# Kernel tuning notes

Measured on AMD Instinct MI355X. Metric: run time of the kernel, lower is better.

Reference implementation:

```python
import jax, jax.numpy as jnp
import numpy as np

B, T, D, H, NW = 2, 2048, 1024, 16, 64
HD = D // H  # 64
EPS = 1e-12  # F.normalize eps


def setup_inputs() -> dict:
    key = jax.random.key(0)
    ks = jax.random.split(key, 8)
    def lin(k, din, dout):
        return jax.random.normal(k, (din, dout), jnp.float32) / np.sqrt(din).astype(np.float32)
    return {
        "x": jax.random.normal(ks[0], (B, T, D), jnp.float32),
        "Wqf": lin(ks[1], D, H * NW), "bqf": jnp.zeros((H * NW,), jnp.float32),
        "Wkf": lin(ks[2], D, H * NW), "bkf": jnp.zeros((H * NW,), jnp.float32),
        "Wqp": lin(ks[3], D, H * NW), "bqp": jnp.zeros((H * NW,), jnp.float32),
        "Wkp": lin(ks[4], D, H * NW), "bkp": jnp.zeros((H * NW,), jnp.float32),
        "Wv": lin(ks[5], D, D), "bv": jnp.zeros((D,), jnp.float32),
        "Wo": lin(ks[6], D, D), "bo": jnp.zeros((D,), jnp.float32),
        "scale": jnp.ones((H, 1, 1), jnp.float32),  # interference_scale
    }


def reference(x, Wqf, bqf, Wkf, bkf, Wqp, bqp, Wkp, bkp, Wv, bv, Wo, bo, scale):
    Bx, Tx, Dx = x.shape
    def heads(W, b, nd):  # [B,T,H*nd] -> [B,H,T,nd]
        return jnp.transpose((x @ W + b).reshape(Bx, Tx, H, nd), (0, 2, 1, 3))
    qf = heads(Wqf, bqf, NW); kf = heads(Wkf, bkf, NW)
    qp = heads(Wqp, bqp, NW); kp = heads(Wkp, bkp, NW)
    v = heads(Wv, bv, HD)
    t = jnp.arange(Tx, dtype=x.dtype)[None, None, :, None]  # [1,1,T,1]
    def wave_norm(f, p):
        w = jnp.sin(f * t + p)  # [B,H,T,NW]
        n = jnp.sqrt(jnp.sum(w * w, axis=-1, keepdims=True))
        return w / jnp.maximum(n, EPS)
    qn = wave_norm(qf, qp)
    kn = wave_norm(kf, kp)
    inter = jnp.einsum('bhtw,bhsw->bhts', qn, kn) * scale[None]  # [B,H,T,T]
    causal = jnp.tril(jnp.ones((Tx, Tx), bool))  # keep diag and below
    inter = jnp.where(causal, inter, jnp.zeros((), x.dtype))
    denom = jnp.sqrt(jnp.arange(1, Tx + 1, dtype=x.dtype))[:, None]  # [T,1]
    attn = inter / denom
    # dropout is identity in eval mode
    out = jnp.einsum('bhts,bhsd->bhtd', attn, v)
    out = jnp.transpose(out, (0, 2, 1, 3)).reshape(Bx, Tx, Dx)
    return out @ Wo + bo
```

## Files before the change

kernel.cpp:

```cpp
#include <hip/hip_runtime.h>


#define Bb 2
#define Tt 2048
#define Dd 1024
#define Hh 16
#define NC 32

typedef _Float16 half_t;
typedef _Float16 half8 __attribute__((ext_vector_type(8)));
typedef _Float16 half4h __attribute__((ext_vector_type(4)));
typedef float f32x16 __attribute__((ext_vector_type(16)));

#define MFMA32(a, b, c) __builtin_amdgcn_mfma_f32_32x32x16_f16((a), (b), (c), 0, 0, 0)

#define GLL(G, L) __builtin_amdgcn_global_load_lds(                      \
    (const __attribute__((address_space(1))) void*)(G),                  \
    (__attribute__((address_space(3))) void*)(L), 16, 0, 0)

__global__ __launch_bounds__(256) void xsplit_kernel(
    const float* __restrict__ X, half_t* __restrict__ XHI, half_t* __restrict__ XLO)
{
  const size_t i = ((size_t)blockIdx.x * 256 + threadIdx.x) * 8;
  float4 a = *(const float4*)&X[i];
  float4 b = *(const float4*)&X[i + 4];
  const float av[8] = {a.x, a.y, a.z, a.w, b.x, b.y, b.z, b.w};
  half8 hv, lv;
  #pragma unroll
  for (int j = 0; j < 8; ++j) {
    half_t hx = (half_t)av[j];
    hv[j] = hx; lv[j] = (half_t)((av[j] - (float)hx) * 2048.f);
  }
  *(half8*)&XHI[i] = hv;
  *(half8*)&XLO[i] = lv;
}

__global__ __launch_bounds__(256) void wsplit_kernel(
    const float* __restrict__ W0, const float* __restrict__ W1,
    const float* __restrict__ W2, const float* __restrict__ W3,
    const float* __restrict__ W4, const float* __restrict__ W5,
    half_t* __restrict__ WSP)
{
  __shared__ float Ld[64][68];
  const int tid = threadIdx.x;
  const int m = blockIdx.z;
  const float* W = (m == 0) ? W0 : (m == 1) ? W1 : (m == 2) ? W2
                 : (m == 3) ? W3 : (m == 4) ? W4 : W5;
  const int k0 = blockIdx.x * 64, n0 = blockIdx.y * 64;
  const int r = tid >> 2, c4 = (tid & 3) * 16;
  #pragma unroll
  for (int i = 0; i < 4; ++i)
    *(float4*)&Ld[r][c4 + i * 4] =
        *(const float4*)&W[(size_t)(k0 + r) * Dd + n0 + c4 + i * 4];
  __syncthreads();
  half_t* hi = WSP + (size_t)m * 2097152;
  half_t* lo = hi + 1048576;
  const int n = tid >> 2, kc = (tid & 3) * 16;
  half8 hv0, hv1, lv0, lv1;
  #pragma unroll
  for (int i = 0; i < 8; ++i) {
    float v0 = Ld[kc + i][n];
    half_t h0 = (half_t)v0;
    hv0[i] = h0; lv0[i] = (half_t)((v0 - (float)h0) * 2048.f);
    float v1 = Ld[kc + 8 + i][n];
    half_t h1 = (half_t)v1;
    hv1[i] = h1; lv1[i] = (half_t)((v1 - (float)h1) * 2048.f);
  }
  *(half8*)&hi[(size_t)(n0 + n) * Dd + k0 + kc]     = hv0;
  *(half8*)&hi[(size_t)(n0 + n) * Dd + k0 + kc + 8] = hv1;
  *(half8*)&lo[(size_t)(n0 + n) * Dd + k0 + kc]     = lv0;
  *(half8*)&lo[(size_t)(n0 + n) * Dd + k0 + kc + 8] = lv1;
}

__global__ __launch_bounds__(256, 2) void proj_kernel(
    const half_t* __restrict__ XHI, const half_t* __restrict__ XLO,
    const half_t* __restrict__ WSP,
    const float* __restrict__ bqf, const float* __restrict__ bqp,
    const float* __restrict__ bkf, const float* __restrict__ bkp,
    half_t* __restrict__ QNH, half_t* __restrict__ KNH)
{
  __shared__ __align__(16) half_t Bs[4][128][64];
  const int tid = threadIdx.x;
  const int mb = blockIdx.x, h = blockIdx.y;
  const int b = blockIdx.z >> 1, p = blockIdx.z & 1;
  const int t0 = mb * 128, row0 = b * Tt + t0, col0 = h * 64;
  const half_t* WF = WSP + (size_t)(2 * p) * 2097152;
  const half_t* WP = WSP + (size_t)(2 * p + 1) * 2097152;
  const float* BF = p ? bkf : bqf;
  const float* BP = p ? bkp : bqp;
  half_t* OUTH = p ? KNH : QNH;

  f32x16 hh[4], mx[4];
  #pragma unroll
  for (int i = 0; i < 4; ++i) { hh[i] = (f32x16)(0.f); mx[i] = (f32x16)(0.f); }

  const int lane = tid & 63, w = tid >> 6;
  const int rl = lane & 31, kq = lane >> 5;
  const int sw = rl & 7;

  const half_t* aHi = XHI + (size_t)(row0 + 32 * w + rl) * Dd + kq * 8;
  const half_t* aLo = XLO + (size_t)(row0 + 32 * w + rl) * Dd + kq * 8;

  const int lr8 = lane >> 3;
  const int lcc = (lane & 7) ^ lr8;
  const int csel = (lcc & 3) * 8;
  const size_t loOff = (lcc >= 4) ? 1048576 : 0;
  const half_t* gb0 = WF + loOff + (size_t)(col0 + 8 * w + lr8) * Dd + csel;
  const half_t* gb1 = gb0 + 32 * Dd;
  const half_t* gb2 = WP + loOff + (size_t)(col0 + 8 * w + lr8) * Dd + csel;
  const half_t* gb3 = gb2 + 32 * Dd;

#define STAGE_PB(BI, K) {                          \
    GLL(gb0 + (K), &Bs[BI][8 * w][0]);             \
    GLL(gb1 + (K), &Bs[BI][32 + 8 * w][0]);        \
    GLL(gb2 + (K), &Bs[BI][64 + 8 * w][0]);        \
    GLL(gb3 + (K), &Bs[BI][96 + 8 * w][0]); }

#define LOADA(H0, H1, L0, L1, K) {                 \
    H0 = *(const half8*)&aHi[(K)];                 \
    H1 = *(const half8*)&aHi[(K) + 16];            \
    L0 = *(const half8*)&aLo[(K)];                 \
    L1 = *(const half8*)&aLo[(K) + 16]; }

#define KT_P(H0, H1, L0, L1, BI) {                                     \
    { const int c0 = (kq ^ sw) * 8, c1 = ((4 + kq) ^ sw) * 8;          \
      _Pragma("unroll")                                                \
      for (int tn = 0; tn < 4; ++tn) {                                 \
        half8 bh = *(const half8*)&Bs[BI][32 * tn + rl][c0];           \
        half8 bl = *(const half8*)&Bs[BI][32 * tn + rl][c1];           \
        hh[tn] = MFMA32(H0, bh, hh[tn]);                               \
        mx[tn] = MFMA32(H0, bl, mx[tn]);                               \
        mx[tn] = MFMA32(L0, bh, mx[tn]); } }                           \
    { const int c0 = (((2 + kq)) ^ sw) * 8, c1 = ((6 + kq) ^ sw) * 8;  \
      _Pragma("unroll")                                                \
      for (int tn = 0; tn < 4; ++tn) {                                 \
        half8 bh = *(const half8*)&Bs[BI][32 * tn + rl][c0];           \
        half8 bl = *(const half8*)&Bs[BI][32 * tn + rl][c1];           \
        hh[tn] = MFMA32(H1, bh, hh[tn]);                               \
        mx[tn] = MFMA32(H1, bl, mx[tn]);                               \
        mx[tn] = MFMA32(L1, bh, mx[tn]); } } }

  half8 pa0, pa1, pa2, pa3, pb0, pb1, pb2, pb3;
  STAGE_PB(0, 0)
  STAGE_PB(1, 32)
  LOADA(pa0, pa1, pa2, pa3, 0)
  __syncthreads();

  #pragma unroll 1
  for (int k0 = 0; k0 < Dd; k0 += 128) {
    if (k0 + 64 < Dd) { STAGE_PB(2, k0 + 64) STAGE_PB(3, k0 + 96) }
    LOADA(pb0, pb1, pb2, pb3, k0 + 32)
    KT_P(pa0, pa1, pa2, pa3, 0)
    if (k0 + 64 < Dd) { LOADA(pa0, pa1, pa2, pa3, k0 + 64) }
    KT_P(pb0, pb1, pb2, pb3, 1)
    __syncthreads();
    if (k0 + 128 < Dd) { STAGE_PB(0, k0 + 128) STAGE_PB(1, k0 + 160) }
    if (k0 + 96 < Dd)  { LOADA(pb0, pb1, pb2, pb3, k0 + 96) }
    KT_P(pa0, pa1, pa2, pa3, 2)
    if (k0 + 128 < Dd) { LOADA(pa0, pa1, pa2, pa3, k0 + 128) }
    KT_P(pb0, pb1, pb2, pb3, 3)
    __syncthreads();
  }
#undef STAGE_PB
#undef LOADA
#undef KT_P

  const float bf0 = BF[col0 + rl], bf1 = BF[col0 + 32 + rl];
  const float bp0 = BP[col0 + rl], bp1 = BP[col0 + 32 + rl];
  #pragma unroll
  for (int j = 0; j < 16; ++j) {
    const int rtj = (j & 3) + 8 * (j >> 2) + 4 * kq;
    const float tf = (float)(t0 + 32 * w + rtj);
    float f0 = hh[0][j] + mx[0][j] * (1.f / 2048.f) + bf0;
    float f1 = hh[1][j] + mx[1][j] * (1.f / 2048.f) + bf1;
    float p0 = hh[2][j] + mx[2][j] * (1.f / 2048.f) + bp0;
    float p1 = hh[3][j] + mx[3][j] * (1.f / 2048.f) + bp1;
    float w0 = sinf(fmaf(f0, tf, p0));
    float w1 = sinf(fmaf(f1, tf, p1));
    float ss = w0 * w0 + w1 * w1;
    ss += __shfl_xor(ss, 1); ss += __shfl_xor(ss, 2);
    ss += __shfl_xor(ss, 4); ss += __shfl_xor(ss, 8);
    ss += __shfl_xor(ss, 16);
    const float inv = 1.f / fmaxf(sqrtf(ss), 1e-12f);
    half_t* op = &OUTH[((size_t)(b * Tt) + t0 + 32 * w + rtj) * Dd + col0];
    op[rl]      = (half_t)(w0 * inv);
    op[32 + rl] = (half_t)(w1 * inv);
  }
}

__global__ __launch_bounds__(256, 2) void gemm_kernel(
    const half_t* __restrict__ AHI, const half_t* __restrict__ ALO,
    const half_t* __restrict__ WHI,
    const float* __restrict__ BIAS, float* __restrict__ OUT)
{
  __shared__ __align__(16) half_t As[2][128][64];
  __shared__ __align__(16) half_t Bs[2][128][64];
  const int tid = threadIdx.x;
  const int m0 = blockIdx.x * 128, n0 = blockIdx.y * 128;

  f32x16 hh[4], mx[4];
  #pragma unroll
  for (int i = 0; i < 4; ++i) { hh[i] = (f32x16)(0.f); mx[i] = (f32x16)(0.f); }

  const int lane = tid & 63, w = tid >> 6;
  const int rl = lane & 31, kq = lane >> 5;
  const int sw = rl & 7;

  const int r = tid & 127, isB = tid >> 7;
  const int swr = r & 7;
  const half_t* srcHi = isB ? &WHI[(size_t)(n0 + r) * Dd]
                            : &AHI[(size_t)(m0 + r) * Dd];
  const half_t* srcLo = isB ? &WHI[1048576 + (size_t)(n0 + r) * Dd]
                            : &ALO[(size_t)(m0 + r) * Dd];
  half_t* dstRow = isB ? &Bs[0][r][0] : &As[0][r][0];
  const int pc0 = (0 ^ swr) * 8, pc1 = (1 ^ swr) * 8;
  const int pc2 = (2 ^ swr) * 8, pc3 = (3 ^ swr) * 8;
  const int pc4 = (4 ^ swr) * 8, pc5 = (5 ^ swr) * 8;
  const int pc6 = (6 ^ swr) * 8, pc7 = (7 ^ swr) * 8;

  half8 rg0, rg1, rg2, rg3, rg4, rg5, rg6, rg7;

#define G_LOADREGS(K)                                                          \
  rg0 = *(const half8*)&srcHi[(K)];      rg1 = *(const half8*)&srcHi[(K) + 8]; \
  rg2 = *(const half8*)&srcHi[(K) + 16]; rg3 = *(const half8*)&srcHi[(K) + 24];\
  rg4 = *(const half8*)&srcLo[(K)];      rg5 = *(const half8*)&srcLo[(K) + 8]; \
  rg6 = *(const half8*)&srcLo[(K) + 16]; rg7 = *(const half8*)&srcLo[(K) + 24];

#define G_WRITE(BI) {                                                     \
  half_t* d_ = dstRow + (BI) * 8192;                                      \
  *(half8*)&d_[pc0] = rg0; *(half8*)&d_[pc1] = rg1;                       \
  *(half8*)&d_[pc2] = rg2; *(half8*)&d_[pc3] = rg3;                       \
  *(half8*)&d_[pc4] = rg4; *(half8*)&d_[pc5] = rg5;                       \
  *(half8*)&d_[pc6] = rg6; *(half8*)&d_[pc7] = rg7; }

#define G_KT(BI)                                                          \
  _Pragma("unroll")                                                       \
  for (int ks = 0; ks < 2; ++ks) {                                        \
    half8 ahi = *(const half8*)&As[BI][32 * w + rl][((2 * ks + kq) ^ sw) * 8];       \
    half8 alo = *(const half8*)&As[BI][32 * w + rl][((4 + 2 * ks + kq) ^ sw) * 8];   \
    _Pragma("unroll")                                                     \
    for (int tn = 0; tn < 4; ++tn) {                                      \
      half8 bhi = *(const half8*)&Bs[BI][32 * tn + rl][((2 * ks + kq) ^ sw) * 8];    \
      half8 blo = *(const half8*)&Bs[BI][32 * tn + rl][((4 + 2 * ks + kq) ^ sw) * 8];\
      hh[tn] = MFMA32(ahi, bhi, hh[tn]);                                  \
      mx[tn] = MFMA32(ahi, blo, mx[tn]);                                  \
      mx[tn] = MFMA32(alo, bhi, mx[tn]);                                  \
    }                                                                     \
  }

  G_LOADREGS(0)
  G_WRITE(0)
  G_LOADREGS(32)
  __syncthreads();

  #pragma unroll 1
  for (int k0 = 0; k0 < Dd; k0 += 64) {
    G_KT(0)
    G_WRITE(1)
    if (k0 + 64 < Dd) { G_LOADREGS(k0 + 64) }
    __syncthreads();
    G_KT(1)
    if (k0 + 64 < Dd) { G_WRITE(0) }
    if (k0 + 96 < Dd) { G_LOADREGS(k0 + 96) }
    __syncthreads();
  }
#undef G_LOADREGS
#undef G_WRITE
#undef G_KT

  const float bb0 = BIAS[n0 + rl],      bb1 = BIAS[n0 + 32 + rl];
  const float bb2 = BIAS[n0 + 64 + rl], bb3 = BIAS[n0 + 96 + rl];
  #pragma unroll
  for (int j = 0; j < 16; ++j) {
    const int rtj = (j & 3) + 8 * (j >> 2) + 4 * kq;
    float* orow = &OUT[(size_t)(m0 + 32 * w + rtj) * Dd + n0];
    orow[rl]      = hh[0][j] + mx[0][j] * (1.f / 2048.f) + bb0;
    orow[32 + rl] = hh[1][j] + mx[1][j] * (1.f / 2048.f) + bb1;
    orow[64 + rl] = hh[2][j] + mx[2][j] * (1.f / 2048.f) + bb2;
    orow[96 + rl] = hh[3][j] + mx[3][j] * (1.f / 2048.f) + bb3;
  }
}

__global__ __launch_bounds__(256) void chunk_kv_kernel(
    const half_t* __restrict__ KNH, const float* __restrict__ V,
    float* __restrict__ G)
{
  __shared__ float Ks[64][64];
  __shared__ float Vs[64][64];
  const int tid = threadIdx.x;
  const int c = blockIdx.x, h = blockIdx.y, b = blockIdx.z;
  const int s0 = c * 64;
  const int lr = tid >> 2, lc = (tid & 3) * 16;
  {
    const half_t* krow = &KNH[(size_t)(b * Tt + s0 + lr) * Dd + h * 64 + lc];
    half8 ka = *(const half8*)&krow[0];
    half8 kb = *(const half8*)&krow[8];
    #pragma unroll
    for (int i = 0; i < 8; ++i) {
      Ks[lr][lc + i] = (float)ka[i];
      Ks[lr][lc + 8 + i] = (float)kb[i];
    }
    const float* vrow = &V[(size_t)(b * Tt + s0 + lr) * Dd + h * 64 + lc];
    #pragma unroll
    for (int i = 0; i < 4; ++i)
      *(float4*)&Vs[lr][lc + i * 4] = *(const float4*)&vrow[i * 4];
  }
  __syncthreads();

  const int ty = tid >> 4, tx = tid & 15;
  float g[4][4] = {{0.f}};
  #pragma unroll 4
  for (int s = 0; s < 64; ++s) {
    float4 kv = *(const float4*)&Ks[s][ty * 4];
    float4 vv = *(const float4*)&Vs[s][tx * 4];
    const float* k_ = (const float*)&kv;
    const float* v_ = (const float*)&vv;
    #pragma unroll
    for (int i = 0; i < 4; ++i)
      #pragma unroll
      for (int j = 0; j < 4; ++j)
        g[i][j] = fmaf(k_[i], v_[j], g[i][j]);
  }
  float* Gp = G + (((size_t)(b * Hh + h) * NC + c) << 12);
  #pragma unroll
  for (int i = 0; i < 4; ++i)
    *(float4*)&Gp[(ty * 4 + i) * 64 + tx * 4] =
        make_float4(g[i][0], g[i][1], g[i][2], g[i][3]);
}

__global__ __launch_bounds__(256) void prefix_kernel(float* __restrict__ G)
{
  const int seg = blockIdx.x, h = blockIdx.y, b = blockIdx.z;
  float* base = G + (((size_t)(b * Hh + h) * NC) << 12) + seg * 256 + threadIdx.x;
  float acc = 0.f;
  #pragma unroll 4
  for (int c = 0; c < NC; ++c) {
    float* p = base + ((size_t)c << 12);
    const float g = *p;
    *p = acc;
    acc += g;
  }
}

__global__ __launch_bounds__(256) void attn_chunk_kernel(
    const half_t* __restrict__ QNH, const half_t* __restrict__ KNH,
    const float* __restrict__ V, const float* __restrict__ M,
    const float* __restrict__ SCALE,
    half_t* __restrict__ ATTHI, half_t* __restrict__ ATTLO)
{
  __shared__ float Qt[64][68];
  __shared__ float Kt[64][68];
  __shared__ float SM[64][68];
  __shared__ float Vs[64][64];
  const int tid = threadIdx.x;
  const int c = blockIdx.x, h = blockIdx.y, b = blockIdx.z;
  const int t0 = c * 64;
  const int lr = tid >> 2, lc = (tid & 3) * 16;
  {
    const half_t* qrow = &QNH[(size_t)(b * Tt + t0 + lr) * Dd + h * 64 + lc];
    const half_t* krow = &KNH[(size_t)(b * Tt + t0 + lr) * Dd + h * 64 + lc];
    half8 qa = *(const half8*)&qrow[0];
    half8 qb = *(const half8*)&qrow[8];
    half8 ka = *(const half8*)&krow[0];
    half8 kb = *(const half8*)&krow[8];
    #pragma unroll
    for (int i = 0; i < 8; ++i) {
      Qt[lc + i][lr] = (float)qa[i];     Qt[lc + 8 + i][lr] = (float)qb[i];
      Kt[lc + i][lr] = (float)ka[i];     Kt[lc + 8 + i][lr] = (float)kb[i];
    }
    const float* vrow = &V[(size_t)(b * Tt + t0 + lr) * Dd + h * 64 + lc];
    const float* mrow = &M[(((size_t)(b * Hh + h) * NC + c) << 12) + lr * 64 + lc];
    #pragma unroll
    for (int i = 0; i < 4; ++i) {
      *(float4*)&Vs[lr][lc + i * 4] = *(const float4*)&vrow[i * 4];
      *(float4*)&SM[lr][lc + i * 4] = *(const float4*)&mrow[i * 4];
    }
  }
  __syncthreads();

  const int ty = tid >> 4, tx = tid & 15;
  float o[4][4] = {{0.f}};
  float sc[4][4] = {{0.f}};

  #pragma unroll 4
  for (int w = 0; w < 64; ++w) {
    float4 qv = *(const float4*)&Qt[w][ty * 4];
    float4 mv = *(const float4*)&SM[w][tx * 4];
    float4 kv = *(const float4*)&Kt[w][tx * 4];
    const float* q_ = (const float*)&qv;
    const float* m_ = (const float*)&mv;
    const float* k_ = (const float*)&kv;
    #pragma unroll
    for (int i = 0; i < 4; ++i) {
      float qq = q_[i];
      #pragma unroll
      for (int j = 0; j < 4; ++j) {
        o[i][j]  = fmaf(qq, m_[j], o[i][j]);
        sc[i][j] = fmaf(qq, k_[j], sc[i][j]);
      }
    }
  }
  __syncthreads();

  #pragma unroll
  for (int i = 0; i < 4; ++i) {
    const int lt = ty * 4 + i;
    #pragma unroll
    for (int j = 0; j < 4; ++j) {
      const int ls = tx * 4 + j;
      SM[ls][lt] = (ls <= lt) ? sc[i][j] : 0.f;
    }
  }
  __syncthreads();

  #pragma unroll 4
  for (int s = 0; s < 64; ++s) {
    float4 sv = *(const float4*)&SM[s][ty * 4];
    float4 vv = *(const float4*)&Vs[s][tx * 4];
    const float* s_ = (const float*)&sv;
    const float* v_ = (const float*)&vv;
    #pragma unroll
    for (int i = 0; i < 4; ++i)
      #pragma unroll
      for (int j = 0; j < 4; ++j)
        o[i][j] = fmaf(s_[i], v_[j], o[i][j]);
  }

  const float sch = SCALE[h];
  #pragma unroll
  for (int i = 0; i < 4; ++i) {
    const int t = t0 + ty * 4 + i;
    const float fac = sch / sqrtf((float)(t + 1));
    half4h hv, lv;
    #pragma unroll
    for (int j = 0; j < 4; ++j) {
      float v = o[i][j] * fac;
      half_t hx = (half_t)v;
      hv[j] = hx; lv[j] = (half_t)((v - (float)hx) * 2048.f);
    }
    *(half4h*)&ATTHI[(size_t)(b * Tt + t) * Dd + h * 64 + tx * 4] = hv;
    *(half4h*)&ATTLO[(size_t)(b * Tt + t) * Dd + h * 64 + tx * 4] = lv;
  }
}

extern "C" void kernel_launch(void* const* d_in, const int* in_sizes, int n_in,
                              void* d_out, int out_size, void* d_ws, size_t ws_size,
                              hipStream_t stream) {
  const float* x   = (const float*)d_in[0];
  const float* Wqf = (const float*)d_in[1];
  const float* bqf = (const float*)d_in[2];
  const float* Wkf = (const float*)d_in[3];
  const float* bkf = (const float*)d_in[4];
  const float* Wqp = (const float*)d_in[5];
  const float* bqp = (const float*)d_in[6];
  const float* Wkp = (const float*)d_in[7];
  const float* bkp = (const float*)d_in[8];
  const float* Wv  = (const float*)d_in[9];
  const float* bv  = (const float*)d_in[10];
  const float* Wo  = (const float*)d_in[11];
  const float* bo  = (const float*)d_in[12];
  const float* scale = (const float*)d_in[13];

  half_t* WSP = (half_t*)d_ws;
  half_t* qnh = WSP + 12582912;
  half_t* knh = qnh + 4194304;
  float*  G   = (float*)(knh + 4194304);
  half_t* xhi = (half_t*)G;
  half_t* xlo = xhi + 4194304;
  float*  vbuf = (float*)d_out;

  xsplit_kernel<<<dim3(2048), 256, 0, stream>>>(x, xhi, xlo);

  wsplit_kernel<<<dim3(16, 16, 6), 256, 0, stream>>>(Wqf, Wqp, Wkf, Wkp, Wv, Wo, WSP);

  proj_kernel<<<dim3(Tt / 128, Hh, Bb * 2), 256, 0, stream>>>(
      xhi, xlo, WSP, bqf, bqp, bkf, bkp, qnh, knh);

  gemm_kernel<<<dim3((Bb * Tt) / 128, Dd / 128), 256, 0, stream>>>(
      xhi, xlo, WSP + (size_t)4 * 2097152, bv, vbuf);

  chunk_kv_kernel<<<dim3(NC, Hh, Bb), 256, 0, stream>>>(knh, vbuf, G);
  prefix_kernel<<<dim3(16, Hh, Bb), 256, 0, stream>>>(G);
  attn_chunk_kernel<<<dim3(NC, Hh, Bb), 256, 0, stream>>>(
      qnh, knh, vbuf, G, scale, qnh , knh );

  gemm_kernel<<<dim3((Bb * Tt) / 128, Dd / 128), 256, 0, stream>>>(
      qnh, knh, WSP + (size_t)5 * 2097152, bo, (float*)d_out);
}
```

Measured before the change: 371.2 us.

## Use partial vmcnt barriers and a double-buffered B pipeline in projection GEMMs

Replaces __syncthreads in the projection and output GEMM loops with explicit s_waitcnt plus s_barrier, fenced with sched_barrier. In proj_kernel, vmcnt(4) waits only for the async global-to-LDS B tiles and leaves the A register prefetch in flight. The output GEMM waits only on lgkmcnt, so its register prefetches are not drained at each barrier. proj_kernel also shrinks from four to two B stages, halving its LDS footprint, at the cost of a shorter prefetch distance. The inline waitcnt counts depend on the order loads are issued, so a compiler reordering would make them fragile.

```diff
diff --git a/kernel.cpp b/kernel.cpp
--- a/kernel.cpp
+++ b/kernel.cpp
@@ -17,6 +17,20 @@
 #define GLL(G, L) __builtin_amdgcn_global_load_lds(                      \
     (const __attribute__((address_space(1))) void*)(G),                  \
     (__attribute__((address_space(3))) void*)(L), 16, 0, 0)
+
+#define SCHED_FENCE() __builtin_amdgcn_sched_barrier(0)
+
+#define BAR_VM(N) {                                                      \
+    SCHED_FENCE();                                                       \
+    asm volatile("s_waitcnt vmcnt(" #N ") lgkmcnt(0)" ::: "memory");     \
+    __builtin_amdgcn_s_barrier();                                        \
+    SCHED_FENCE(); }
+
+#define BAR_LG() {                                                       \
+    SCHED_FENCE();                                                       \
+    asm volatile("s_waitcnt lgkmcnt(0)" ::: "memory");                   \
+    __builtin_amdgcn_s_barrier();                                        \
+    SCHED_FENCE(); }
 
 __global__ __launch_bounds__(256) void xsplit_kernel(
     const float* __restrict__ X, half_t* __restrict__ XHI, half_t* __restrict__ XLO)
@@ -79,7 +93,7 @@
     const float* __restrict__ bkf, const float* __restrict__ bkp,
     half_t* __restrict__ QNH, half_t* __restrict__ KNH)
 {
-  __shared__ __align__(16) half_t Bs[4][128][64];
+  __shared__ __align__(16) half_t Bs[2][128][64];
   const int tid = threadIdx.x;
   const int mb = blockIdx.x, h = blockIdx.y;
   const int b = blockIdx.z >> 1, p = blockIdx.z & 1;
@@ -114,7 +128,8 @@
     GLL(gb0 + (K), &Bs[BI][8 * w][0]);             \
     GLL(gb1 + (K), &Bs[BI][32 + 8 * w][0]);        \
     GLL(gb2 + (K), &Bs[BI][64 + 8 * w][0]);        \
-    GLL(gb3 + (K), &Bs[BI][96 + 8 * w][0]); }
+    GLL(gb3 + (K), &Bs[BI][96 + 8 * w][0]);        \
+    SCHED_FENCE(); }
 
 #define LOADA(H0, H1, L0, L1, K) {                 \
     H0 = *(const half8*)&aHi[(K)];                 \
@@ -140,26 +155,19 @@
         mx[tn] = MFMA32(H1, bl, mx[tn]);                               \
         mx[tn] = MFMA32(L1, bh, mx[tn]); } } }
 
-  half8 pa0, pa1, pa2, pa3, pb0, pb1, pb2, pb3;
+  half8 ah0c, ah1c, al0c, al1c, ah0n, ah1n, al0n, al1n;
   STAGE_PB(0, 0)
-  STAGE_PB(1, 32)
-  LOADA(pa0, pa1, pa2, pa3, 0)
-  __syncthreads();
+  LOADA(ah0c, ah1c, al0c, al1c, 0)
+  BAR_VM(4)
 
   #pragma unroll 1
-  for (int k0 = 0; k0 < Dd; k0 += 128) {
-    if (k0 + 64 < Dd) { STAGE_PB(2, k0 + 64) STAGE_PB(3, k0 + 96) }
-    LOADA(pb0, pb1, pb2, pb3, k0 + 32)
-    KT_P(pa0, pa1, pa2, pa3, 0)
-    if (k0 + 64 < Dd) { LOADA(pa0, pa1, pa2, pa3, k0 + 64) }
-    KT_P(pb0, pb1, pb2, pb3, 1)
-    __syncthreads();
-    if (k0 + 128 < Dd) { STAGE_PB(0, k0 + 128) STAGE_PB(1, k0 + 160) }
-    if (k0 + 96 < Dd)  { LOADA(pb0, pb1, pb2, pb3, k0 + 96) }
-    KT_P(pa0, pa1, pa2, pa3, 2)
-    if (k0 + 128 < Dd) { LOADA(pa0, pa1, pa2, pa3, k0 + 128) }
-    KT_P(pb0, pb1, pb2, pb3, 3)
-    __syncthreads();
+  for (int k0 = 0; k0 < Dd; k0 += 64) {
+    if (k0 + 32 < Dd) { STAGE_PB(1, k0 + 32) LOADA(ah0n, ah1n, al0n, al1n, k0 + 32) }
+    KT_P(ah0c, ah1c, al0c, al1c, 0)
+    BAR_VM(4)
+    if (k0 + 64 < Dd) { STAGE_PB(0, k0 + 64) LOADA(ah0c, ah1c, al0c, al1c, k0 + 64) }
+    KT_P(ah0n, ah1n, al0n, al1n, 1)
+    BAR_VM(4)
   }
 #undef STAGE_PB
 #undef LOADA
@@ -251,18 +259,18 @@
   G_LOADREGS(0)
   G_WRITE(0)
   G_LOADREGS(32)
-  __syncthreads();
+  BAR_LG()
 
   #pragma unroll 1
   for (int k0 = 0; k0 < Dd; k0 += 64) {
     G_KT(0)
     G_WRITE(1)
     if (k0 + 64 < Dd) { G_LOADREGS(k0 + 64) }
-    __syncthreads();
+    BAR_LG()
     G_KT(1)
     if (k0 + 64 < Dd) { G_WRITE(0) }
     if (k0 + 96 < Dd) { G_LOADREGS(k0 + 96) }
-    __syncthreads();
+    BAR_LG()
   }
 #undef G_LOADREGS
 #undef G_WRITE
```

Measured after the change: 373.6 us. Within noise of the previous version (+0.7%).
